# Kernel tuning notes

Hardware: AMD Instinct MI355X
Metric: run time of the kernel (lower is better)

Reference implementation:

```python
import jax, jax.numpy as jnp
import numpy as np

D_WIN = 4  # local_size (max displacement); (2*D_WIN+1)^2 = 81 displacements


def avg_pool4(x):
    B, C, H, W = x.shape
    return x.reshape(B, C, H // 4, 4, W // 4, 4).mean(axis=(3, 5))


def corr_max(cur, feats, d):
    """FlowNet-style correlation (kernel=1, pad=d, max_disp=d), then max over displacements.
    cur, feats: (B,C,H,W) -> (B,H,W)."""
    B, C, H, W = cur.shape
    p = jnp.pad(feats, ((0, 0), (0, 0), (d, d), (d, d)))
    best = jnp.full((B, H, W), -jnp.inf, cur.dtype)
    for dy in range(2 * d + 1):          # small fixed 81-iteration loop
        for dx in range(2 * d + 1):
            corr = (cur * p[:, :, dy:dy + H, dx:dx + W]).sum(axis=1) / C
            best = jnp.maximum(best, corr)
    return best


def conv2d(x, w, b):
    y = jax.lax.conv_general_dilated(x, w, (1, 1), 'SAME',
                                     dimension_numbers=('NCHW', 'OIHW', 'NCHW'))
    return y + b[None, :, None, None]


def setup_inputs() -> dict:
    key = jax.random.key(0)
    ks = jax.random.split(key, 10)
    B, C, D, H, W = 8, 256, 256, 96, 96
    return {
        'cur_embed':  jax.random.normal(ks[0], (B, C, H, W), jnp.float32),
        'cur_decode': jax.random.normal(ks[1], (B, D, H, W), jnp.float32),
        'init_embed': jax.random.normal(ks[2], (B, C, H, W), jnp.float32),
        'init_seg':   jax.random.uniform(ks[3], (B, 2, H, W), jnp.float32),
        'prev_embed': jax.random.normal(ks[4], (B, C, H, W), jnp.float32),
        'prev_seg':   jax.random.uniform(ks[5], (B, 2, H, W), jnp.float32),
        'W1': jax.random.normal(ks[6], (128, 264, 3, 3), jnp.float32) * 0.02,
        'b1': jnp.zeros((128,), jnp.float32),
        'W2': jax.random.normal(ks[7], (2, 128, 3, 3), jnp.float32) * 0.02,
        'b2': jnp.zeros((2,), jnp.float32),
    }


def reference(cur_embed, cur_decode, init_embed, init_seg, prev_embed, prev_seg,
              W1, b1, W2, b2):
    B, C, H, W = cur_embed.shape
    # ---- global map: per-batch 1x1-conv similarity against pooled init feats ----
    fi = avg_pool4(init_embed)                       # (B,C,h,w)
    si = avg_pool4(init_seg)                         # (B,2,h,w)
    hw = fi.shape[2] * fi.shape[3]
    sim = jnp.einsum('bck,bchw->bkhw', fi.reshape(B, C, hw), cur_embed)  # (B,hw,H,W)
    gmap = jnp.max(sim[:, None] * si.reshape(B, 2, hw)[..., None, None], axis=2)  # (B,2,H,W)
    # ---- local map: windowed cross-correlation against masked prev feats ----
    bg = corr_max(cur_embed, prev_embed * prev_seg[:, 0:1], D_WIN)
    fg = corr_max(cur_embed, prev_embed * prev_seg[:, 1:2], D_WIN)
    lmap = jnp.stack([bg, fg], axis=1)               # (B,2,H,W)
    # ---- merge CNN ----
    h = jnp.concatenate([cur_decode, gmap, init_seg, lmap, prev_seg], axis=1)  # (B,264,H,W)
    h = jax.nn.relu(conv2d(h, W1, b1))
    out = conv2d(h, W2, b2)                          # (B,2,H,W)
    return out
```

## Files before the change

### kernel.cpp

```cpp
#include <hip/hip_runtime.h>
#include <hip/hip_bf16.h>


typedef __hip_bfloat16 bf16;
typedef __attribute__((ext_vector_type(8))) short short8;
typedef __attribute__((ext_vector_type(4))) float f32x4;

constexpr int B_  = 8;
constexpr int C_  = 256;
constexpr int H_  = 96;
constexpr int W_  = 96;
constexpr int HW_ = H_ * W_;
constexpr int PW_ = 24;
constexpr int KP_ = 576;
constexpr int KPP = 640;
constexpr int HP_ = 98;
constexpr int HPW = HP_ * HP_;
constexpr int C1O = 128;
constexpr int CHK = HPW * 32;

__device__ __forceinline__ unsigned short bfb(float f) {
    bf16 h = __float2bfloat16(f);
    return *reinterpret_cast<unsigned short*>(&h);
}

__device__ __forceinline__ void gload_lds16(const bf16* g, bf16* l) {
    __builtin_amdgcn_global_load_lds((const void*)g, (void*)l, 16, 0, 0);
}

__global__ __launch_bounds__(256)
void w1cvt_kernel(const float* __restrict__ W1, bf16* __restrict__ w1bf)
{
    int idx = blockIdx.x * 256 + threadIdx.x;
    if (idx >= 82 * 128 * 32) return;
    int ic = idx & 31;
    int oc = (idx >> 5) & 127;
    int ks = idx >> 12;
    int icc = ks / 9, tap = ks % 9;
    int icg = icc * 32 + ic;
    float v = (icg < 264) ? W1[((size_t)oc * 264 + icg) * 9 + tap] : 0.f;
    w1bf[idx] = __float2bfloat16(v);
}

__global__ __launch_bounds__(256)
void w2cvt_kernel(const float* __restrict__ W2, bf16* __restrict__ w2bf)
{
    int idx = blockIdx.x * 256 + threadIdx.x;
    if (idx >= 18 * 16 * 64) return;
    int c  = idx & 63;
    int oc = (idx >> 6) & 15;
    int s  = idx >> 10;
    int tap = s >> 1, half = s & 1;
    float v = (oc < 2) ? W2[((size_t)oc * 128 + half * 64 + c) * 9 + tap] : 0.f;
    w2bf[idx] = __float2bfloat16(v);
}

__global__ __launch_bounds__(256)
void tcur_kernel(const float* __restrict__ cur, bf16* __restrict__ curbf)
{
    __shared__ float tile[64][68];
    int b = blockIdx.z, c0 = blockIdx.y * 64, p0 = blockIdx.x * 64;
    int t = threadIdx.x;
    const float* src = cur + ((size_t)b * C_ + c0) * HW_ + p0;
    #pragma unroll
    for (int it = 0; it < 4; it++) {
        int f = t + it * 256;
        int cl = f >> 4, p4 = (f & 15) * 4;
        float4 v = *reinterpret_cast<const float4*>(src + (size_t)cl * HW_ + p4);
        *reinterpret_cast<float4*>(&tile[cl][p4]) = v;
    }
    __syncthreads();
    bf16* dst = curbf + ((size_t)b * HW_ + p0) * 256 + c0;
    #pragma unroll
    for (int it = 0; it < 4; it++) {
        int f = t + it * 256;
        int pl = f >> 4, c4 = (f & 15) * 4;
        ushort4 u;
        u.x = bfb(tile[c4 + 0][pl]); u.y = bfb(tile[c4 + 1][pl]);
        u.z = bfb(tile[c4 + 2][pl]); u.w = bfb(tile[c4 + 3][pl]);
        *reinterpret_cast<ushort4*>(dst + (size_t)pl * 256 + c4) = u;
    }
}

__global__ __launch_bounds__(256)
void pool_kernel(const float* __restrict__ init_embed,
                 const float* __restrict__ init_seg,
                 bf16* __restrict__ fibf, float* __restrict__ si)
{
    int idx = blockIdx.x * 256 + threadIdx.x;
    int total = B_ * (C_ + 2) * KPP;
    if (idx >= total) return;
    int k  = idx % KPP;
    int ch = (idx / KPP) % (C_ + 2);
    int b  = idx / (KPP * (C_ + 2));
    float s = 0.f;
    if (k < KP_) {
        int ph = k / PW_, pw = k % PW_;
        const float* src = (ch < C_)
            ? (init_embed + (((size_t)b * C_ + ch) * H_ + ph * 4) * W_ + pw * 4)
            : (init_seg   + (((size_t)b * 2 + (ch - C_)) * H_ + ph * 4) * W_ + pw * 4);
        #pragma unroll
        for (int r = 0; r < 4; r++) {
            float4 v = *reinterpret_cast<const float4*>(src + r * W_);
            s += v.x + v.y + v.z + v.w;
        }
        s *= (1.f / 16.f);
    }
    if (ch < C_) fibf[((size_t)b * KPP + k) * C_ + ch] = __float2bfloat16(s);
    else         si[(size_t)b * 2 * KPP + (ch - C_) * KPP + k] = s;
}

__global__ __launch_bounds__(256)
void gmap_mfma(const bf16* __restrict__ curbf, const bf16* __restrict__ fibf,
               const float* __restrict__ si, float* __restrict__ gout)
{
    __shared__ bf16 Abuf[8192];
    __shared__ bf16 Bbuf[8192];
    __shared__ float bred[2][2][2][64];
    int gid = blockIdx.x;
    int b = gid & 7;
    int p0 = (gid >> 3) * 128;
    int tid = threadIdx.x, lane = tid & 63;
    int w = tid >> 6, wm = w & 1, wn = w >> 1;
    int l15 = lane & 15, lk = lane >> 4;
    const bf16* fb = fibf + (size_t)b * KPP * 256;
    const bf16* cb = curbf + (size_t)b * HW_ * 256;
    const float* sib = si + (size_t)b * 2 * KPP;

    int wbase = tid & 192;
    int t3 = (tid >> 3) & 7;
    int cX = (tid & 7) ^ t3;
    int r0 = tid >> 3;
    int swzE0 = ((lk) ^ (l15 & 7)) * 8;
    int swzE1 = ((4 + lk) ^ (l15 & 7)) * 8;

    float best[2][4];
    #pragma unroll
    for (int s = 0; s < 2; s++)
        #pragma unroll
        for (int nt = 0; nt < 4; nt++) best[s][nt] = -INFINITY;
    f32x4 acc[4][4] = {};

    auto STAGE = [&](int q) {
        int chunk = q >> 2, ks = q & 3;
        int koff = ks * 64 + cX * 8;
        #pragma unroll
        for (int i = 0; i < 4; i++) {
            int row = i * 32 + r0;
            gload_lds16(fb + (size_t)(chunk * 128 + row) * 256 + koff,
                        &Abuf[(size_t)(i * 256 + wbase) * 8]);
            gload_lds16(cb + (size_t)(p0 + row) * 256 + koff,
                        &Bbuf[(size_t)(i * 256 + wbase) * 8]);
        }
    };

    auto COMPUTE = [&]() {
        #pragma unroll
        for (int k = 0; k < 2; k++) {
            int swz = k ? swzE1 : swzE0;
            short8 a[4], bq[4];
            #pragma unroll
            for (int mt = 0; mt < 4; mt++)
                a[mt] = *reinterpret_cast<const short8*>(
                    &Abuf[(size_t)(wm * 64 + mt * 16 + l15) * 64 + swz]);
            #pragma unroll
            for (int nt = 0; nt < 4; nt++)
                bq[nt] = *reinterpret_cast<const short8*>(
                    &Bbuf[(size_t)(wn * 64 + nt * 16 + l15) * 64 + swz]);
            #pragma unroll
            for (int mt = 0; mt < 4; mt++)
                #pragma unroll
                for (int nt = 0; nt < 4; nt++)
                    acc[mt][nt] = __builtin_amdgcn_mfma_f32_16x16x32_bf16(
                        a[mt], bq[nt], acc[mt][nt], 0, 0, 0);
        }
    };

    for (int q = 0; q < 20; ++q) {
        STAGE(q);
        __syncthreads();
        COMPUTE();
        if ((q & 3) == 3) {
            int kp0 = (q >> 2) * 128;
            #pragma unroll
            for (int mt = 0; mt < 4; mt++) {
                int rb = kp0 + wm * 64 + mt * 16 + lk * 4;
                float4 s0 = *reinterpret_cast<const float4*>(sib + rb);
                float4 s1 = *reinterpret_cast<const float4*>(sib + KPP + rb);
                const float* s0p = reinterpret_cast<const float*>(&s0);
                const float* s1p = reinterpret_cast<const float*>(&s1);
                #pragma unroll
                for (int nt = 0; nt < 4; nt++) {
                    #pragma unroll
                    for (int r = 0; r < 4; r++) {
                        float v = acc[mt][nt][r];
                        best[0][nt] = fmaxf(best[0][nt], v * s0p[r]);
                        best[1][nt] = fmaxf(best[1][nt], v * s1p[r]);
                    }
                    acc[mt][nt] = (f32x4){0.f, 0.f, 0.f, 0.f};
                }
            }
        }
        __syncthreads();
    }
    #pragma unroll
    for (int s = 0; s < 2; s++)
        #pragma unroll
        for (int nt = 0; nt < 4; nt++) {
            float v = best[s][nt];
            v = fmaxf(v, __shfl_xor(v, 16));
            v = fmaxf(v, __shfl_xor(v, 32));
            if (lk == 0) bred[wm][wn][s][nt * 16 + l15] = v;
        }
    __syncthreads();
    {
        int wn2 = tid >> 7, s2 = (tid >> 6) & 1, pxl = tid & 63;
        float v = fmaxf(bred[0][wn2][s2][pxl], bred[1][wn2][s2][pxl]);
        gout[((size_t)b * 2 + s2) * HW_ + p0 + wn2 * 64 + pxl] = v;
    }
}

__global__ __launch_bounds__(256)
void lmap_mfma(const bf16* __restrict__ curbf, const bf16* __restrict__ prevbf,
               const bf16* __restrict__ zbuf,
               const float* __restrict__ prev_seg, float* __restrict__ lout, int b0)
{
    constexpr int GSTR = 257;
    constexpr int SEGB = 64 * GSTR;
    constexpr int REDB = SEGB + 512;
    __shared__ __align__(16) char Smem[(REDB + 256) * 4];
    bf16* Abuf = (bf16*)Smem;
    bf16* Bbuf = (bf16*)(Smem + 8192);
    float* gl  = (float*)Smem;

    int b = b0 + blockIdx.y;
    const bf16* pb = prevbf + (size_t)blockIdx.y * HW_ * 256;
    const bf16* cb = curbf + (size_t)b * HW_ * 256;
    int tile = blockIdx.x;
    int ty0 = (tile / 12) * 8, tx0 = (tile % 12) * 8;
    int tid = threadIdx.x, lane = tid & 63, wn = tid >> 6;
    int l15 = lane & 15, lk = lane >> 4;

    int wbase = tid & 192;
    int t3 = (tid >> 3) & 7;
    int cX = (tid & 7) ^ t3;
    int r0 = tid >> 3;
    int swzE0 = ((lk) ^ (l15 & 7)) * 8;
    int swzE1 = ((4 + lk) ^ (l15 & 7)) * 8;

    int gpxA0 = (ty0 + (r0 >> 3)) * W_ + tx0 + (r0 & 7);
    int gpxA1 = (ty0 + (r0 >> 3) + 4) * W_ + tx0 + (r0 & 7);
    const bf16* rowB[8];
    #pragma unroll
    for (int i = 0; i < 8; i++) {
        int wrow = i * 32 + r0;
        int wy = wrow >> 4, wx = wrow & 15;
        int gy = ty0 - 4 + wy, gx = tx0 - 4 + wx;
        bool ok = (gy >= 0) && (gy < H_) && (gx >= 0) && (gx < W_);
        rowB[i] = ok ? (pb + (size_t)(gy * W_ + gx) * 256) : zbuf;
    }

    f32x4 acc[4][4] = {};

    for (int ks = 0; ks < 4; ++ks) {
        int koff = ks * 64 + cX * 8;
        gload_lds16(cb + (size_t)gpxA0 * 256 + koff, &Abuf[(size_t)(wbase) * 8]);
        gload_lds16(cb + (size_t)gpxA1 * 256 + koff, &Abuf[(size_t)(256 + wbase) * 8]);
        #pragma unroll
        for (int i = 0; i < 8; i++)
            gload_lds16(rowB[i] + koff, &Bbuf[(size_t)(i * 256 + wbase) * 8]);
        __syncthreads();
        #pragma unroll
        for (int k = 0; k < 2; k++) {
            int swz = k ? swzE1 : swzE0;
            short8 a[4], bq[4];
            #pragma unroll
            for (int mt = 0; mt < 4; mt++)
                a[mt] = *reinterpret_cast<const short8*>(
                    &Abuf[(size_t)(mt * 16 + l15) * 64 + swz]);
            #pragma unroll
            for (int nt = 0; nt < 4; nt++)
                bq[nt] = *reinterpret_cast<const short8*>(
                    &Bbuf[(size_t)(wn * 64 + nt * 16 + l15) * 64 + swz]);
            #pragma unroll
            for (int mt = 0; mt < 4; mt++)
                #pragma unroll
                for (int nt = 0; nt < 4; nt++)
                    acc[mt][nt] = __builtin_amdgcn_mfma_f32_16x16x32_bf16(
                        a[mt], bq[nt], acc[mt][nt], 0, 0, 0);
        }
        __syncthreads();
    }

    #pragma unroll
    for (int mt = 0; mt < 4; mt++)
        #pragma unroll
        for (int nt = 0; nt < 4; nt++)
            #pragma unroll
            for (int r = 0; r < 4; r++)
                gl[(mt * 16 + lk * 4 + r) * GSTR + wn * 64 + nt * 16 + l15] = acc[mt][nt][r];
    #pragma unroll
    for (int it = 0; it < 2; it++) {
        int f = tid + it * 256;
        int s = f >> 8, wp = f & 255;
        int wy = wp >> 4, wx = wp & 15;
        int gy = ty0 - 4 + wy, gxx = tx0 - 4 + wx;
        float v = 0.f;
        if (gy >= 0 && gy < H_ && gxx >= 0 && gxx < W_)
            v = prev_seg[((size_t)b * 2 + s) * HW_ + gy * W_ + gxx] * (1.f / 256.f);
        gl[SEGB + f] = v;
    }
    __syncthreads();
    {
        int m = tid & 63;
        int sh = tid >> 6;
        int s = sh >> 1, hh = sh & 1;
        int py = m >> 3, lx = m & 7;
        const float* gr = gl + m * GSTR;
        const float* sr = gl + SEGB + s * 256;
        float mx = -INFINITY;
        int wr0 = hh * 5, wr1 = hh ? 9 : 5;
        for (int wr = wr0; wr < wr1; ++wr) {
            int base = (py + wr) * 16 + lx;
            #pragma unroll
            for (int wc = 0; wc < 9; ++wc)
                mx = fmaxf(mx, gr[base + wc] * sr[base + wc]);
        }
        gl[REDB + sh * 64 + m] = mx;
    }
    __syncthreads();
    if (tid < 128) {
        int s = tid >> 6, m = tid & 63;
        float v = fmaxf(gl[REDB + (s * 2 + 0) * 64 + m], gl[REDB + (s * 2 + 1) * 64 + m]);
        int gpx = (ty0 + (m >> 3)) * W_ + tx0 + (m & 7);
        lout[((size_t)b * 2 + s) * HW_ + gpx] = v;
    }
}

__global__ __launch_bounds__(256)
void pack_dec_kernel(const float* __restrict__ dec, bf16* __restrict__ hcat8)
{
    __shared__ float tile[64][68];
    int b = blockIdx.z, c0 = blockIdx.y * 64, p0 = blockIdx.x * 64;
    int t = threadIdx.x;
    const float* src = dec + ((size_t)b * C_ + c0) * HW_ + p0;
    #pragma unroll
    for (int it = 0; it < 4; it++) {
        int f = t + it * 256;
        int cl = f >> 4, p4 = (f & 15) * 4;
        float4 v = *reinterpret_cast<const float4*>(src + (size_t)cl * HW_ + p4);
        *reinterpret_cast<float4*>(&tile[cl][p4]) = v;
    }
    __syncthreads();
    #pragma unroll
    for (int it = 0; it < 4; it++) {
        int f = t + it * 256;
        int pl = f >> 4, c4 = (f & 15) * 4;
        int p = p0 + pl;
        int y = p / 96, x = p % 96;
        int pos = (y + 1) * HP_ + x + 1;
        int ch = c0 + c4;
        ushort4 u;
        u.x = bfb(tile[c4 + 0][pl]); u.y = bfb(tile[c4 + 1][pl]);
        u.z = bfb(tile[c4 + 2][pl]); u.w = bfb(tile[c4 + 3][pl]);
        bf16* dst = hcat8 + ((size_t)b * 8 + (ch >> 5)) * CHK + (size_t)pos * 32 + (ch & 31);
        *reinterpret_cast<ushort4*>(dst) = u;
    }
}

__global__ __launch_bounds__(256)
void pack_small_kernel(const float* __restrict__ gout,
                       const float* __restrict__ lout,
                       const float* __restrict__ init_seg,
                       const float* __restrict__ prev_seg,
                       bf16* __restrict__ hcat1)
{
    int idx = blockIdx.x * 256 + threadIdx.x;
    if (idx >= B_ * HW_) return;
    int b = idx / HW_, p = idx % HW_;
    int y = p / 96, x = p % 96;
    int pos = (y + 1) * HP_ + x + 1;
    bf16* dst = hcat1 + ((size_t)b * HPW + pos) * 8;
    float g0 = gout[((size_t)b * 2 + 0) * HW_ + p];
    float g1 = gout[((size_t)b * 2 + 1) * HW_ + p];
    float i0 = init_seg[((size_t)b * 2 + 0) * HW_ + p];
    float i1 = init_seg[((size_t)b * 2 + 1) * HW_ + p];
    float l0 = lout[((size_t)b * 2 + 0) * HW_ + p];
    float l1 = lout[((size_t)b * 2 + 1) * HW_ + p];
    float q0 = prev_seg[((size_t)b * 2 + 0) * HW_ + p];
    float q1 = prev_seg[((size_t)b * 2 + 1) * HW_ + p];
    ushort4 u; u.x = bfb(g0); u.y = bfb(g1); u.z = bfb(i0); u.w = bfb(i1);
    *reinterpret_cast<ushort4*>(dst) = u;
    ushort4 u2; u2.x = bfb(l0); u2.y = bfb(l1); u2.z = bfb(q0); u2.w = bfb(q1);
    *reinterpret_cast<ushort4*>(dst + 4) = u2;
}

__global__ __launch_bounds__(256)
void zero_border_kernel(bf16* __restrict__ hcat8, bf16* __restrict__ hcat1,
                        bf16* __restrict__ hmidp)
{
    int idx = blockIdx.x * 256 + threadIdx.x;
    if (idx >= B_ * 388) return;
    int b = idx / 388, bi = idx % 388;
    int pos;
    if (bi < 98) pos = bi;
    else if (bi < 196) pos = 97 * HP_ + (bi - 98);
    else if (bi < 292) pos = (bi - 196 + 1) * HP_;
    else pos = (bi - 292 + 1) * HP_ + 97;
    const short8 Z = {0, 0, 0, 0, 0, 0, 0, 0};
    #pragma unroll
    for (int c = 0; c < 8; c++) {
        bf16* p = hcat8 + ((size_t)b * 8 + c) * CHK + (size_t)pos * 32;
        #pragma unroll
        for (int j = 0; j < 4; j++)
            *reinterpret_cast<short8*>(p + j * 8) = Z;
    }
    *reinterpret_cast<short8*>(hcat1 + ((size_t)b * HPW + pos) * 8) = Z;
    bf16* q = hmidp + ((size_t)b * HPW + pos) * 128;
    #pragma unroll
    for (int j = 0; j < 16; j++)
        *reinterpret_cast<short8*>(q + j * 8) = Z;
}

__global__ __launch_bounds__(256)
void conv1_mfma(const bf16* __restrict__ hcat8, const bf16* __restrict__ hcat1,
                const bf16* __restrict__ w1bf, const float* __restrict__ b1,
                bf16* __restrict__ hmidp)
{
    __shared__ bf16 S[14336];
    bf16* Abuf = S;
    bf16* Bbuf = S + 8192;
    int gid = blockIdx.x;
    int b = gid & 7;
    int row = gid >> 3;
    int tid = threadIdx.x, lane = tid & 63;
    int w = tid >> 6, wm = w & 1, wn = w >> 1;
    int l15 = lane & 15, lk = lane >> 4;
    const bf16* hb8 = hcat8 + (size_t)b * 8 * CHK;
    const bf16* hb1 = hcat1 + (size_t)b * HPW * 8;

    int wbase = tid & 192;
    int t3 = (tid >> 3) & 7;
    int cX = (tid & 7) ^ t3;
    int selX = cX >> 2;
    int cin8 = (cX & 3) * 8;
    int r0 = tid >> 3;
    int swzE0 = ((lk) ^ (l15 & 7)) * 8;
    int swzE1 = ((4 + lk) ^ (l15 & 7)) * 8;

    f32x4 acc[4][3] = {};

    auto STAGE = [&](int p) {
        int s0 = 2 * p, s1 = s0 + 1;
        int icc0 = s0 / 9, tap0 = s0 - icc0 * 9;
        int icc1 = s1 / 9, tap1 = s1 - icc1 * 9;
        const bf16* gA = w1bf + (size_t)p * 8192 + (size_t)selX * 4096 + cin8;
        #pragma unroll
        for (int i = 0; i < 4; i++)
            gload_lds16(gA + (i * 32 + r0) * 32,
                        &Abuf[(size_t)(i * 256 + wbase) * 8]);
        int tapS = selX ? tap1 : tap0;
        int iccS = selX ? icc1 : icc0;
        int posT = (row + tapS / 3) * HP_ + (tapS % 3);
        bool is8 = (iccS >= 8);
        const bf16* gb = is8 ? hb1 : (hb8 + (size_t)iccS * CHK);
        #pragma unroll
        for (int i = 0; i < 3; i++) {
            int c = i * 32 + r0;
            const bf16* g = is8 ? (gb + (size_t)(posT + c) * 8)
                                : (gb + (size_t)(posT + c) * 32 + cin8);
            gload_lds16(g, &Bbuf[(size_t)(i * 256 + wbase) * 8]);
        }
    };

    auto COMPUTE = [&]() {
        #pragma unroll
        for (int k = 0; k < 2; k++) {
            int swz = k ? swzE1 : swzE0;
            short8 a[4], bq[3];
            #pragma unroll
            for (int mt = 0; mt < 4; mt++)
                a[mt] = *reinterpret_cast<const short8*>(
                    &Abuf[(size_t)(wm * 64 + mt * 16 + l15) * 64 + swz]);
            #pragma unroll
            for (int nt = 0; nt < 3; nt++)
                bq[nt] = *reinterpret_cast<const short8*>(
                    &Bbuf[(size_t)(wn * 48 + nt * 16 + l15) * 64 + swz]);
            #pragma unroll
            for (int mt = 0; mt < 4; mt++)
                #pragma unroll
                for (int nt = 0; nt < 3; nt++)
                    acc[mt][nt] = __builtin_amdgcn_mfma_f32_16x16x32_bf16(
                        a[mt], bq[nt], acc[mt][nt], 0, 0, 0);
        }
    };

    for (int p = 0; p < 41; ++p) {
        STAGE(p);
        __syncthreads();
        COMPUTE();
        __syncthreads();
    }

    #pragma unroll
    for (int nt = 0; nt < 3; nt++) {
        int pxl = wn * 48 + nt * 16 + l15;
        #pragma unroll
        for (int mt = 0; mt < 4; mt++) {
            int ocb = wm * 64 + mt * 16 + lk * 4;
            float4 bias = *reinterpret_cast<const float4*>(b1 + ocb);
            const float* bp = reinterpret_cast<const float*>(&bias);
            ushort4 u;
            u.x = bfb(fmaxf(acc[mt][nt][0] + bp[0], 0.f));
            u.y = bfb(fmaxf(acc[mt][nt][1] + bp[1], 0.f));
            u.z = bfb(fmaxf(acc[mt][nt][2] + bp[2], 0.f));
            u.w = bfb(fmaxf(acc[mt][nt][3] + bp[3], 0.f));
            int chunk = (ocb >> 3) ^ (pxl & 7);
            *reinterpret_cast<ushort4*>(&S[(size_t)pxl * 128 + chunk * 8 + (lk & 1) * 4]) = u;
        }
    }
    __syncthreads();
    {
        bf16* dst = hmidp + (size_t)b * HPW * 128 + ((size_t)(row + 1) * HP_ + 1) * 128;
        #pragma unroll
        for (int i = 0; i < 6; i++) {
            int f = tid + i * 256;
            int px = f >> 4, cc = f & 15;
            short8 v = *reinterpret_cast<const short8*>(
                &S[(size_t)px * 128 + (cc ^ (px & 7)) * 8]);
            *reinterpret_cast<short8*>(dst + (size_t)f * 8) = v;
        }
    }
}

__global__ __launch_bounds__(256)
void conv2_mfma(const bf16* __restrict__ hmidp, const bf16* __restrict__ w2bf,
                const float* __restrict__ b2, float* __restrict__ out)
{
    __shared__ bf16 Abuf[1024];
    __shared__ bf16 Bbuf[8192];
    int gid = blockIdx.x;
    int b = gid & 7;
    int p0 = (gid >> 3) * 128;
    int tid = threadIdx.x, lane = tid & 63;
    int wn = tid >> 6;
    int l15 = lane & 15, lk = lane >> 4;
    const bf16* hb = hmidp + (size_t)b * HPW * 128;

    int wbase = tid & 192;
    int t3 = (tid >> 3) & 7;
    int cX = (tid & 7) ^ t3;
    int r0 = tid >> 3;
    int posB[4];
    #pragma unroll
    for (int i = 0; i < 4; i++) {
        int px = p0 + i * 32 + r0;
        posB[i] = (px / 96) * HP_ + (px % 96);
    }
    int swzE0 = ((lk) ^ (l15 & 7)) * 8;
    int swzE1 = ((4 + lk) ^ (l15 & 7)) * 8;

    f32x4 acc[2] = {};

    auto STAGE = [&](int s) {
        int tap = s >> 1, half = s & 1;
        int toff = (tap / 3) * HP_ + (tap % 3);
        if (tid < 128)
            gload_lds16(w2bf + ((size_t)s * 16 + r0) * 64 + cX * 8,
                        &Abuf[(size_t)(tid & 192) * 8]);
        #pragma unroll
        for (int i = 0; i < 4; i++)
            gload_lds16(hb + (size_t)(posB[i] + toff) * 128 + half * 64 + cX * 8,
                        &Bbuf[(size_t)(i * 256 + wbase) * 8]);
    };

    auto COMPUTE = [&]() {
        #pragma unroll
        for (int k = 0; k < 2; k++) {
            int swz = k ? swzE1 : swzE0;
            short8 a = *reinterpret_cast<const short8*>(&Abuf[(size_t)l15 * 64 + swz]);
            #pragma unroll
            for (int nt = 0; nt < 2; nt++) {
                short8 bq = *reinterpret_cast<const short8*>(
                    &Bbuf[(size_t)(wn * 32 + nt * 16 + l15) * 64 + swz]);
                acc[nt] = __builtin_amdgcn_mfma_f32_16x16x32_bf16(a, bq, acc[nt], 0, 0, 0);
            }
        }
    };

    for (int s = 0; s < 18; ++s) {
        STAGE(s);
        __syncthreads();
        COMPUTE();
        __syncthreads();
    }

    if (lk == 0) {
        float bb0 = b2[0], bb1 = b2[1];
        #pragma unroll
        for (int nt = 0; nt < 2; nt++) {
            int px = p0 + wn * 32 + nt * 16 + l15;
            out[((size_t)b * 2 + 0) * HW_ + px] = acc[nt][0] + bb0;
            out[((size_t)b * 2 + 1) * HW_ + px] = acc[nt][1] + bb1;
        }
    }
}

extern "C" void kernel_launch(void* const* d_in, const int* in_sizes, int n_in,
                              void* d_out, int out_size, void* d_ws, size_t ws_size,
                              hipStream_t stream)
{
    const float* cur_embed  = (const float*)d_in[0];
    const float* cur_decode = (const float*)d_in[1];
    const float* init_embed = (const float*)d_in[2];
    const float* init_seg   = (const float*)d_in[3];
    const float* prev_embed = (const float*)d_in[4];
    const float* prev_seg   = (const float*)d_in[5];
    const float* W1 = (const float*)d_in[6];
    const float* b1 = (const float*)d_in[7];
    const float* W2 = (const float*)d_in[8];
    const float* b2 = (const float*)d_in[9];
    float* out = (float*)d_out;

    char* ws = (char*)d_ws;
    bf16* hcat8 = (bf16*)ws;
    bf16* curbf = (bf16*)ws;
    bf16* hcat1 = (bf16*)(ws + 39337984);
    const size_t HCAT_REGION = 40567296;
    bf16* hmidp  = (bf16*)(ws + HCAT_REGION);
    bf16* fibf   = (bf16*)(ws + HCAT_REGION);
    bf16* prevbf = (bf16*)(ws + HCAT_REGION);
    float* si  = (float*)(ws + HCAT_REGION + 2621440);
    bf16* w1bf = (bf16*)(ws + 60236288);
    bf16* w2bf = (bf16*)(ws + 60908032);
    float* gout = (float*)(ws + 60944896);
    float* lout = (float*)(ws + 61534720);
    const bf16* zbuf = w1bf + (size_t)81 * 4096;

    { int total = 82 * 128 * 32;
      w1cvt_kernel<<<(total + 255) / 256, 256, 0, stream>>>(W1, w1bf); }
    { int total = 18 * 16 * 64;
      w2cvt_kernel<<<(total + 255) / 256, 256, 0, stream>>>(W2, w2bf); }
    { dim3 g(144, 4, B_);
      tcur_kernel<<<g, 256, 0, stream>>>(cur_embed, curbf); }
    { int total = B_ * (C_ + 2) * KPP;
      pool_kernel<<<(total + 255) / 256, 256, 0, stream>>>(init_embed, init_seg, fibf, si); }
    { gmap_mfma<<<576, 256, 0, stream>>>(curbf, fibf, si, gout); }
    for (int g = 0; g < 2; g++) {
        dim3 gt(144, 4, 4);
        tcur_kernel<<<gt, 256, 0, stream>>>(prev_embed + (size_t)g * 4 * C_ * HW_, prevbf);
        dim3 gl(144, 4);
        lmap_mfma<<<gl, 256, 0, stream>>>(curbf, prevbf, zbuf, prev_seg, lout, g * 4);
    }
    { int total = B_ * 388;
      zero_border_kernel<<<(total + 255) / 256, 256, 0, stream>>>(hcat8, hcat1, hmidp); }
    { dim3 g(144, 4, B_);
      pack_dec_kernel<<<g, 256, 0, stream>>>(cur_decode, hcat8); }
    { int total = B_ * HW_;
      pack_small_kernel<<<(total + 255) / 256, 256, 0, stream>>>(gout, lout, init_seg, prev_seg, hcat1); }
    { conv1_mfma<<<768, 256, 0, stream>>>(hcat8, hcat1, w1bf, b1, hmidp); }
    { conv2_mfma<<<576, 256, 0, stream>>>(hmidp, w2bf, b2, out); }
}
```

Before: 264.1 us.

## Retile gmap and conv2 to 96-pixel tiles and merge weight conversion kernels

gmap_mfma now processes 96 pixels per block instead of 128, which raises the grid from 576 to 768 blocks so it fills more CUs. conv2_mfma is retiled to one image row of 96 pixels per block with 128 threads and 768 blocks, which drops the per-pixel padded-position arithmetic. The two weight-conversion kernels are fused into one launch. The trade-off is less reuse of each staged A tile per block and a lower MFMA-to-load ratio.

```diff
diff --git a/kernel.cpp b/kernel.cpp
--- a/kernel.cpp
+++ b/kernel.cpp
@@ -29,30 +29,28 @@
 }
 
 __global__ __launch_bounds__(256)
-void w1cvt_kernel(const float* __restrict__ W1, bf16* __restrict__ w1bf)
+void wcvt_kernel(const float* __restrict__ W1, const float* __restrict__ W2,
+                 bf16* __restrict__ w1bf, bf16* __restrict__ w2bf)
 {
     int idx = blockIdx.x * 256 + threadIdx.x;
-    if (idx >= 82 * 128 * 32) return;
-    int ic = idx & 31;
-    int oc = (idx >> 5) & 127;
-    int ks = idx >> 12;
-    int icc = ks / 9, tap = ks % 9;
-    int icg = icc * 32 + ic;
-    float v = (icg < 264) ? W1[((size_t)oc * 264 + icg) * 9 + tap] : 0.f;
-    w1bf[idx] = __float2bfloat16(v);
-}
-
-__global__ __launch_bounds__(256)
-void w2cvt_kernel(const float* __restrict__ W2, bf16* __restrict__ w2bf)
-{
-    int idx = blockIdx.x * 256 + threadIdx.x;
-    if (idx >= 18 * 16 * 64) return;
-    int c  = idx & 63;
-    int oc = (idx >> 6) & 15;
-    int s  = idx >> 10;
-    int tap = s >> 1, half = s & 1;
-    float v = (oc < 2) ? W2[((size_t)oc * 128 + half * 64 + c) * 9 + tap] : 0.f;
-    w2bf[idx] = __float2bfloat16(v);
+    if (idx < 82 * 128 * 32) {
+        int ic = idx & 31;
+        int oc = (idx >> 5) & 127;
+        int ks = idx >> 12;
+        int icc = ks / 9, tap = ks % 9;
+        int icg = icc * 32 + ic;
+        float v = (icg < 264) ? W1[((size_t)oc * 264 + icg) * 9 + tap] : 0.f;
+        w1bf[idx] = __float2bfloat16(v);
+    } else {
+        int j = idx - 82 * 128 * 32;
+        if (j >= 18 * 16 * 64) return;
+        int c  = j & 63;
+        int oc = (j >> 6) & 15;
+        int s  = j >> 10;
+        int tap = s >> 1, half = s & 1;
+        float v = (oc < 2) ? W2[((size_t)oc * 128 + half * 64 + c) * 9 + tap] : 0.f;
+        w2bf[j] = __float2bfloat16(v);
+    }
 }
 
 __global__ __launch_bounds__(256)
@@ -115,11 +113,11 @@
                const float* __restrict__ si, float* __restrict__ gout)
 {
     __shared__ bf16 Abuf[8192];
-    __shared__ bf16 Bbuf[8192];
-    __shared__ float bred[2][2][2][64];
+    __shared__ bf16 Bbuf[6144];
+    __shared__ float bred[2][2][2][48];
     int gid = blockIdx.x;
     int b = gid & 7;
-    int p0 = (gid >> 3) * 128;
+    int p0 = (gid >> 3) * 96;
     int tid = threadIdx.x, lane = tid & 63;
     int w = tid >> 6, wm = w & 1, wn = w >> 1;
     int l15 = lane & 15, lk = lane >> 4;
@@ -134,12 +132,12 @@
     int swzE0 = ((lk) ^ (l15 & 7)) * 8;
     int swzE1 = ((4 + lk) ^ (l15 & 7)) * 8;
 
-    float best[2][4];
+    float best[2][3];
     #pragma unroll
     for (int s = 0; s < 2; s++)
         #pragma unroll
-        for (int nt = 0; nt < 4; nt++) best[s][nt] = -INFINITY;
-    f32x4 acc[4][4] = {};
+        for (int nt = 0; nt < 3; nt++) best[s][nt] = -INFINITY;
+    f32x4 acc[4][3] = {};
 
     auto STAGE = [&](int q) {
         int chunk = q >> 2, ks = q & 3;
@@ -149,6 +147,10 @@
             int row = i * 32 + r0;
             gload_lds16(fb + (size_t)(chunk * 128 + row) * 256 + koff,
                         &Abuf[(size_t)(i * 256 + wbase) * 8]);
+        }
+        #pragma unroll
+        for (int i = 0; i < 3; i++) {
+            int row = i * 32 + r0;
             gload_lds16(cb + (size_t)(p0 + row) * 256 + koff,
                         &Bbuf[(size_t)(i * 256 + wbase) * 8]);
         }
@@ -158,19 +160,19 @@
         #pragma unroll
         for (int k = 0; k < 2; k++) {
             int swz = k ? swzE1 : swzE0;
-            short8 a[4], bq[4];
+            short8 a[4], bq[3];
             #pragma unroll
             for (int mt = 0; mt < 4; mt++)
                 a[mt] = *reinterpret_cast<const short8*>(
                     &Abuf[(size_t)(wm * 64 + mt * 16 + l15) * 64 + swz]);
             #pragma unroll
-            for (int nt = 0; nt < 4; nt++)
+            for (int nt = 0; nt < 3; nt++)
                 bq[nt] = *reinterpret_cast<const short8*>(
-                    &Bbuf[(size_t)(wn * 64 + nt * 16 + l15) * 64 + swz]);
+                    &Bbuf[(size_t)(wn * 48 + nt * 16 + l15) * 64 + swz]);
             #pragma unroll
             for (int mt = 0; mt < 4; mt++)
                 #pragma unroll
-                for (int nt = 0; nt < 4; nt++)
+                for (int nt = 0; nt < 3; nt++)
                     acc[mt][nt] = __builtin_amdgcn_mfma_f32_16x16x32_bf16(
                         a[mt], bq[nt], acc[mt][nt], 0, 0, 0);
         }
@@ -190,7 +192,7 @@
                 const float* s0p = reinterpret_cast<const float*>(&s0);
                 const float* s1p = reinterpret_cast<const float*>(&s1);
                 #pragma unroll
-                for (int nt = 0; nt < 4; nt++) {
+                for (int nt = 0; nt < 3; nt++) {
                     #pragma unroll
                     for (int r = 0; r < 4; r++) {
                         float v = acc[mt][nt][r];
@@ -206,17 +208,18 @@
     #pragma unroll
     for (int s = 0; s < 2; s++)
         #pragma unroll
-        for (int nt = 0; nt < 4; nt++) {
+        for (int nt = 0; nt < 3; nt++) {
             float v = best[s][nt];
             v = fmaxf(v, __shfl_xor(v, 16));
             v = fmaxf(v, __shfl_xor(v, 32));
             if (lk == 0) bred[wm][wn][s][nt * 16 + l15] = v;
         }
     __syncthreads();
-    {
-        int wn2 = tid >> 7, s2 = (tid >> 6) & 1, pxl = tid & 63;
-        float v = fmaxf(bred[0][wn2][s2][pxl], bred[1][wn2][s2][pxl]);
-        gout[((size_t)b * 2 + s2) * HW_ + p0 + wn2 * 64 + pxl] = v;
+    if (tid < 192) {
+        int s2 = tid / 96, pxl = tid % 96;
+        float v = fmaxf(bred[0][pxl / 48][s2][pxl % 48],
+                        bred[1][pxl / 48][s2][pxl % 48]);
+        gout[((size_t)b * 2 + s2) * HW_ + p0 + pxl] = v;
     }
 }
 
@@ -533,45 +536,41 @@
     }
 }
 
-__global__ __launch_bounds__(256)
+__global__ __launch_bounds__(128)
 void conv2_mfma(const bf16* __restrict__ hmidp, const bf16* __restrict__ w2bf,
                 const float* __restrict__ b2, float* __restrict__ out)
 {
     __shared__ bf16 Abuf[1024];
-    __shared__ bf16 Bbuf[8192];
+    __shared__ bf16 Bbuf[6144];
     int gid = blockIdx.x;
     int b = gid & 7;
-    int p0 = (gid >> 3) * 128;
+    int y = gid >> 3;
+    int p0 = y * 96;
     int tid = threadIdx.x, lane = tid & 63;
     int wn = tid >> 6;
     int l15 = lane & 15, lk = lane >> 4;
     const bf16* hb = hmidp + (size_t)b * HPW * 128;
 
-    int wbase = tid & 192;
+    int wbase = tid & 64;
     int t3 = (tid >> 3) & 7;
     int cX = (tid & 7) ^ t3;
     int r0 = tid >> 3;
-    int posB[4];
-    #pragma unroll
-    for (int i = 0; i < 4; i++) {
-        int px = p0 + i * 32 + r0;
-        posB[i] = (px / 96) * HP_ + (px % 96);
-    }
     int swzE0 = ((lk) ^ (l15 & 7)) * 8;
     int swzE1 = ((4 + lk) ^ (l15 & 7)) * 8;
 
-    f32x4 acc[2] = {};
+    f32x4 acc[3] = {};
 
     auto STAGE = [&](int s) {
         int tap = s >> 1, half = s & 1;
         int toff = (tap / 3) * HP_ + (tap % 3);
-        if (tid < 128)
-            gload_lds16(w2bf + ((size_t)s * 16 + r0) * 64 + cX * 8,
-                        &Abuf[(size_t)(tid & 192) * 8]);
-        #pragma unroll
-        for (int i = 0; i < 4; i++)
-            gload_lds16(hb + (size_t)(posB[i] + toff) * 128 + half * 64 + cX * 8,
-                        &Bbuf[(size_t)(i * 256 + wbase) * 8]);
+        gload_lds16(w2bf + ((size_t)s * 16 + r0) * 64 + cX * 8,
+                    &Abuf[(size_t)wbase * 8]);
+        #pragma unroll
+        for (int i = 0; i < 6; i++) {
+            int c = i * 16 + r0;
+            gload_lds16(hb + (size_t)(y * HP_ + c + toff) * 128 + half * 64 + cX * 8,
+                        &Bbuf[(size_t)(i * 128 + wbase) * 8]);
+        }
     };
 
     auto COMPUTE = [&]() {
@@ -580,9 +579,9 @@
             int swz = k ? swzE1 : swzE0;
             short8 a = *reinterpret_cast<const short8*>(&Abuf[(size_t)l15 * 64 + swz]);
             #pragma unroll
-            for (int nt = 0; nt < 2; nt++) {
+            for (int nt = 0; nt < 3; nt++) {
                 short8 bq = *reinterpret_cast<const short8*>(
-                    &Bbuf[(size_t)(wn * 32 + nt * 16 + l15) * 64 + swz]);
+                    &Bbuf[(size_t)(wn * 48 + nt * 16 + l15) * 64 + swz]);
                 acc[nt] = __builtin_amdgcn_mfma_f32_16x16x32_bf16(a, bq, acc[nt], 0, 0, 0);
             }
         }
@@ -598,8 +597,8 @@
     if (lk == 0) {
         float bb0 = b2[0], bb1 = b2[1];
         #pragma unroll
-        for (int nt = 0; nt < 2; nt++) {
-            int px = p0 + wn * 32 + nt * 16 + l15;
+        for (int nt = 0; nt < 3; nt++) {
+            int px = p0 + wn * 48 + nt * 16 + l15;
             out[((size_t)b * 2 + 0) * HW_ + px] = acc[nt][0] + bb0;
             out[((size_t)b * 2 + 1) * HW_ + px] = acc[nt][1] + bb1;
         }
@@ -637,15 +636,13 @@
     float* lout = (float*)(ws + 61534720);
     const bf16* zbuf = w1bf + (size_t)81 * 4096;
 
-    { int total = 82 * 128 * 32;
-      w1cvt_kernel<<<(total + 255) / 256, 256, 0, stream>>>(W1, w1bf); }
-    { int total = 18 * 16 * 64;
-      w2cvt_kernel<<<(total + 255) / 256, 256, 0, stream>>>(W2, w2bf); }
+    { int total = 82 * 128 * 32 + 18 * 16 * 64;
+      wcvt_kernel<<<(total + 255) / 256, 256, 0, stream>>>(W1, W2, w1bf, w2bf); }
     { dim3 g(144, 4, B_);
       tcur_kernel<<<g, 256, 0, stream>>>(cur_embed, curbf); }
     { int total = B_ * (C_ + 2) * KPP;
       pool_kernel<<<(total + 255) / 256, 256, 0, stream>>>(init_embed, init_seg, fibf, si); }
-    { gmap_mfma<<<576, 256, 0, stream>>>(curbf, fibf, si, gout); }
+    { gmap_mfma<<<768, 256, 0, stream>>>(curbf, fibf, si, gout); }
     for (int g = 0; g < 2; g++) {
         dim3 gt(144, 4, 4);
         tcur_kernel<<<gt, 256, 0, stream>>>(prev_embed + (size_t)g * 4 * C_ * HW_, prevbf);
@@ -659,5 +656,5 @@
     { int total = B_ * HW_;
       pack_small_kernel<<<(total + 255) / 256, 256, 0, stream>>>(gout, lout, init_seg, prev_seg, hcat1); }
     { conv1_mfma<<<768, 256, 0, stream>>>(hcat8, hcat1, w1bf, b1, hmidp); }
-    { conv2_mfma<<<576, 256, 0, stream>>>(hmidp, w2bf, b2, out); }
-}
+    { conv2_mfma<<<768, 128, 0, stream>>>(hmidp, w2bf, b2, out); }
+}
```

New measurement: 253.3 us. 1.04x faster.
